# Performance work log

Hardware: AMD Instinct MI355X
Metric: run time of the kernel (lower is better)

The kernel has to match this reference:

```python
import jax, jax.numpy as jnp
import numpy as np

N_NODES = 50000
N_EDGES = 1600000
D_FEAT = 128
EMB = 32
HEADS = 4
SLOPE = 0.2  # PyG GATv2 default negative_slope


def setup_inputs() -> dict:
    key = jax.random.key(0)
    ks = jax.random.split(key, 12)
    H, C = HEADS, EMB
    hid = H * C  # concat output dim = 128

    def glorot(k, shape):
        fan_in, fan_out = shape[0], shape[-1] if len(shape) > 1 else shape[0]
        lim = jnp.sqrt(6.0 / (fan_in + fan_out)).astype(jnp.float32)
        return jax.random.uniform(k, shape, jnp.float32, -lim, lim)

    x = jax.random.normal(ks[0], (N_NODES, D_FEAT), jnp.float32)
    edge_index = jax.random.randint(ks[1], (2, N_EDGES), 0, N_NODES, jnp.int32).astype(jnp.int64)

    return {
        "x": x,
        "edge_index": edge_index,
        # layer 1: in D_FEAT -> H*C (separate source/target lins, share_weights=False)
        "W1_l": glorot(ks[2], (D_FEAT, hid)),
        "W1_r": glorot(ks[3], (D_FEAT, hid)),
        "att1": glorot(ks[4], (H, C)),
        "b1": jnp.zeros((hid,), jnp.float32),
        # layer 2: in H*C -> H*C
        "W2_l": glorot(ks[5], (hid, hid)),
        "W2_r": glorot(ks[6], (hid, hid)),
        "att2": glorot(ks[7], (H, C)),
        "b2": jnp.zeros((hid,), jnp.float32),
    }


def _gatv2_layer(x, src, dst, W_l, W_r, att, bias, n_nodes):
    H, C = att.shape
    xl = (x @ W_l).reshape(n_nodes, H, C)  # source-side transform
    xr = (x @ W_r).reshape(n_nodes, H, C)  # target-side transform
    # per-edge pre-activation: GATv2 applies LeakyReLU BEFORE the attention dot
    msg = xl[src] + xr[dst]                               # [E, H, C]
    e = jnp.einsum('ehc,hc->eh', jax.nn.leaky_relu(msg, SLOPE), att)  # [E, H]
    # numerically stable segment softmax over incoming edges of each dst node
    m = jax.ops.segment_max(e, dst, num_segments=n_nodes)  # [N, H]
    ex = jnp.exp(e - m[dst])
    denom = jax.ops.segment_sum(ex, dst, num_segments=n_nodes)  # [N, H]
    alpha = ex / (denom[dst] + 1e-16)                     # [E, H]
    out = jax.ops.segment_sum(alpha[:, :, None] * xl[src], dst, num_segments=n_nodes)
    return out.reshape(n_nodes, H * C) + bias


def reference(x, edge_index, W1_l, W1_r, att1, b1, W2_l, W2_r, att2, b2):
    n = x.shape[0]
    # PyG default add_self_loops=True: append (i -> i) for every node
    loop = jnp.arange(n, dtype=edge_index.dtype)
    src = jnp.concatenate([edge_index[0], loop])
    dst = jnp.concatenate([edge_index[1], loop])
    h = jax.nn.relu(_gatv2_layer(x, src, dst, W1_l, W1_r, att1, b1, n))
    h = jax.nn.relu(_gatv2_layer(h, src, dst, W2_l, W2_r, att2, b2, n))
    return h
```

## Files before the change

kernel.cpp:

```cpp
#include <hip/hip_runtime.h>

#define N_NODES 50000
#define N_EDGES 1600000
#define ET (N_EDGES + N_NODES)
#define DF 128
#define SLOPE 0.2f

#define NB 196
#define BCAP 10240
#define P1_CHUNK 4096

typedef __attribute__((ext_vector_type(8))) short bf16x8;
typedef __attribute__((ext_vector_type(4))) float floatx4;
typedef __attribute__((ext_vector_type(8))) _Float16 half8;
typedef __attribute__((ext_vector_type(2))) _Float16 half2v;

__device__ inline unsigned short f2bf(float v) {
    unsigned int u = __float_as_uint(v);
    u += 0x7FFF + ((u >> 16) & 1);
    return (unsigned short)(u >> 16);
}
__device__ inline void splitbf(float v, unsigned short& h, unsigned short& l) {
    h = f2bf(v);
    float hf = __uint_as_float((unsigned int)h << 16);
    l = f2bf(v - hf);
}

__global__ __launch_bounds__(256) void bin_wconv(
    const int* __restrict__ ei,
    const float* __restrict__ W0, const float* __restrict__ W1,
    const float* __restrict__ W2, const float* __restrict__ W3,
    unsigned short* __restrict__ Wh, unsigned short* __restrict__ Wl,
    int* __restrict__ g_count, int* __restrict__ bucket_mem)
{
    const int tid = threadIdx.x;
    if (blockIdx.x < 256) {
        int idx = blockIdx.x * 256 + tid;
        int m = idx >> 14, rem = idx & 16383;
        const float* W = (m == 0) ? W0 : (m == 1) ? W1 : (m == 2) ? W2 : W3;
        int c = rem >> 7, k = rem & 127;
        unsigned short h, l;
        splitbf(W[k * 128 + c], h, l);
        Wh[(size_t)m * 16384 + c * 128 + k] = h;
        Wl[(size_t)m * 16384 + c * 128 + k] = l;
    }

    __shared__ int cnt[NB], base[NB], cnt2[NB];
    for (int i = tid; i < NB; i += 256) { cnt[i] = 0; cnt2[i] = 0; }
    __syncthreads();

    const int e0 = blockIdx.x * P1_CHUNK;
    int srcv[16], dstv[16];
#pragma unroll
    for (int i = 0; i < 16; i++) {
        int eid = e0 + i * 256 + tid;
        int s = 0, d = -1;
        if (eid < ET) {
            if (eid < N_EDGES) { s = ei[eid]; d = ei[N_EDGES + eid]; }
            else               { s = d = eid - N_EDGES; }
        }
        srcv[i] = s; dstv[i] = d;
        if (d >= 0) atomicAdd(&cnt[d >> 8], 1);
    }
    __syncthreads();
    for (int i = tid; i < NB; i += 256)
        base[i] = (cnt[i] > 0) ? atomicAdd(&g_count[i], cnt[i]) : 0;
    __syncthreads();
#pragma unroll
    for (int i = 0; i < 16; i++) {
        int d = dstv[i];
        if (d >= 0) {
            int b = d >> 8;
            int r = atomicAdd(&cnt2[b], 1);
            int slot = base[b] + r;
            if (slot < BCAP)
                bucket_mem[(size_t)b * BCAP + slot] =
                    (srcv[i] & 0xFFFF) | ((d & 255) << 16);
        }
    }
}

__global__ __launch_bounds__(256) void csr_pass(const int* __restrict__ g_count,
                                                const int* __restrict__ bucket_mem,
                                                int* __restrict__ row_ptr,
                                                unsigned short* __restrict__ csr_src)
{
    __shared__ int sh_edges[BCAP];
    __shared__ int hist[256], offs[256], excl[256], cnt2[256];
    __shared__ int gsc[256];
    const int b = blockIdx.x, tid = threadIdx.x;

    gsc[tid] = (tid < NB) ? g_count[tid] : 0;
    __syncthreads();
    for (int d = 1; d < 256; d <<= 1) {
        int x = (tid >= d) ? gsc[tid - d] : 0;
        __syncthreads();
        gsc[tid] += x;
        __syncthreads();
    }
    const int base_csr = (b > 0) ? gsc[b - 1] : 0;

    int m = g_count[b]; if (m > BCAP) m = BCAP;
    hist[tid] = 0; cnt2[tid] = 0;
    __syncthreads();
    const int* bm = bucket_mem + (size_t)b * BCAP;
    for (int i = tid; i < m; i += 256) {
        int p = bm[i];
        sh_edges[i] = p;
        atomicAdd(&hist[(p >> 16) & 255], 1);
    }
    __syncthreads();
    offs[tid] = hist[tid]; __syncthreads();
    for (int d = 1; d < 256; d <<= 1) {
        int x = (tid >= d) ? offs[tid - d] : 0;
        __syncthreads();
        offs[tid] += x;
        __syncthreads();
    }
    excl[tid] = offs[tid] - hist[tid];
    const int node0 = b << 8;
    if (node0 + tid < N_NODES) row_ptr[node0 + tid] = base_csr + excl[tid];
    if (b == 0 && tid == 0) row_ptr[N_NODES] = ET;
    __syncthreads();
    for (int i = tid; i < m; i += 256) {
        int p = sh_edges[i];
        int dl = (p >> 16) & 255;
        int r = atomicAdd(&cnt2[dl], 1);
        csr_src[base_csr + excl[dl] + r] = (unsigned short)(p & 0xFFFF);
    }
}

__global__ __launch_bounds__(256) void gemm_mfma(
    const float* __restrict__ X,
    const unsigned short* __restrict__ WhL, const unsigned short* __restrict__ WlL,
    const unsigned short* __restrict__ WhR, const unsigned short* __restrict__ WlR,
    _Float16* __restrict__ outL, _Float16* __restrict__ outR, int M)
{
    __shared__ unsigned short xh[64 * 40], xl[64 * 40];
    __shared__ unsigned short whL[128 * 40], wlL[128 * 40];
    __shared__ unsigned short whR[128 * 40], wlR[128 * 40];

    const int t = threadIdx.x;
    const int row0 = blockIdx.x * 64;
    const int lane = t & 63, wv = t >> 6;
    const int lm = lane & 15, quad = lane >> 4;
    const int m0 = wv * 16;

    floatx4 accL[8], accR[8];
#pragma unroll
    for (int i = 0; i < 8; i++) { accL[i] = (floatx4)0.f; accR[i] = (floatx4)0.f; }

    const int sr = t >> 2;
    const int sc = (t & 3) * 8;
    const int wn = t >> 1;
    const int wkh = (t & 1) * 16;

    for (int kb = 0; kb < 128; kb += 32) {
        int xrow = row0 + sr; if (xrow >= M) xrow = M - 1;
        const float* xp = X + (size_t)xrow * DF + kb + sc;
        float4 v0 = *(const float4*)(xp);
        float4 v1 = *(const float4*)(xp + 4);
        ushort4 h0, h1, l0, l1;
        splitbf(v0.x, h0.x, l0.x); splitbf(v0.y, h0.y, l0.y);
        splitbf(v0.z, h0.z, l0.z); splitbf(v0.w, h0.w, l0.w);
        splitbf(v1.x, h1.x, l1.x); splitbf(v1.y, h1.y, l1.y);
        splitbf(v1.z, h1.z, l1.z); splitbf(v1.w, h1.w, l1.w);
        *(ushort4*)&xh[sr * 40 + sc]     = h0;
        *(ushort4*)&xh[sr * 40 + sc + 4] = h1;
        *(ushort4*)&xl[sr * 40 + sc]     = l0;
        *(ushort4*)&xl[sr * 40 + sc + 4] = l1;

        const size_t wofs = (size_t)wn * 128 + kb + wkh;
        {
            const uint4* p = (const uint4*)(WhL + wofs);
            uint4 a = p[0], b = p[1];
            *(uint4*)&whL[wn * 40 + wkh] = a; *(uint4*)&whL[wn * 40 + wkh + 8] = b;
        }
        {
            const uint4* p = (const uint4*)(WlL + wofs);
            uint4 a = p[0], b = p[1];
            *(uint4*)&wlL[wn * 40 + wkh] = a; *(uint4*)&wlL[wn * 40 + wkh + 8] = b;
        }
        {
            const uint4* p = (const uint4*)(WhR + wofs);
            uint4 a = p[0], b = p[1];
            *(uint4*)&whR[wn * 40 + wkh] = a; *(uint4*)&whR[wn * 40 + wkh + 8] = b;
        }
        {
            const uint4* p = (const uint4*)(WlR + wofs);
            uint4 a = p[0], b = p[1];
            *(uint4*)&wlR[wn * 40 + wkh] = a; *(uint4*)&wlR[wn * 40 + wkh + 8] = b;
        }
        __syncthreads();

        bf16x8 ahf = *(const bf16x8*)&xh[(m0 + lm) * 40 + quad * 8];
        bf16x8 alf = *(const bf16x8*)&xl[(m0 + lm) * 40 + quad * 8];
#pragma unroll
        for (int nt = 0; nt < 8; nt++) {
            const int bofs = (nt * 16 + lm) * 40 + quad * 8;
            bf16x8 bh = *(const bf16x8*)&whL[bofs];
            bf16x8 bl = *(const bf16x8*)&wlL[bofs];
            accL[nt] = __builtin_amdgcn_mfma_f32_16x16x32_bf16(ahf, bh, accL[nt], 0, 0, 0);
            accL[nt] = __builtin_amdgcn_mfma_f32_16x16x32_bf16(ahf, bl, accL[nt], 0, 0, 0);
            accL[nt] = __builtin_amdgcn_mfma_f32_16x16x32_bf16(alf, bh, accL[nt], 0, 0, 0);
            bf16x8 ch = *(const bf16x8*)&whR[bofs];
            bf16x8 cl = *(const bf16x8*)&wlR[bofs];
            accR[nt] = __builtin_amdgcn_mfma_f32_16x16x32_bf16(ahf, ch, accR[nt], 0, 0, 0);
            accR[nt] = __builtin_amdgcn_mfma_f32_16x16x32_bf16(ahf, cl, accR[nt], 0, 0, 0);
            accR[nt] = __builtin_amdgcn_mfma_f32_16x16x32_bf16(alf, ch, accR[nt], 0, 0, 0);
        }
        __syncthreads();
    }

#pragma unroll
    for (int nt = 0; nt < 8; nt++) {
        int col = (nt >> 2) * 64 + (nt & 3) * 16 + lm;
#pragma unroll
        for (int r = 0; r < 4; r++) {
            int gr = row0 + m0 + quad * 4 + r;
            if (gr < M) {
                size_t o = (size_t)gr * DF + col;
                outL[o] = (_Float16)accL[nt][r];
                outR[o] = (_Float16)accR[nt][r];
            }
        }
    }
}

__global__ __launch_bounds__(256) void fused_agg(
    const _Float16* __restrict__ XL, const _Float16* __restrict__ XR,
    const int* __restrict__ row_ptr, const unsigned short* __restrict__ csr_src,
    const float* __restrict__ att, const float* __restrict__ bias,
    float* __restrict__ out)
{
    const int t = threadIdx.x;
    const int wave = t >> 6, l = t & 63;
    const int g = l >> 4, gl = l & 15;
    const int n = blockIdx.x * 4 + wave;
    if (n >= N_NODES) return;
    const int beg = row_ptr[n], end = row_ptr[n + 1];

    const int c0 = gl * 8;
    half8 xrh = *(const half8*)(XR + (size_t)n * DF + c0);
    float4 at0 = *(const float4*)(att + c0);
    float4 at1 = *(const float4*)(att + c0 + 4);
    half2v a01 = { (_Float16)at0.x, (_Float16)at0.y };
    half2v a23 = { (_Float16)at0.z, (_Float16)at0.w };
    half2v a45 = { (_Float16)at1.x, (_Float16)at1.y };
    half2v a67 = { (_Float16)at1.z, (_Float16)at1.w };
    const half8 slp = { (_Float16)SLOPE, (_Float16)SLOPE, (_Float16)SLOPE, (_Float16)SLOPE,
                        (_Float16)SLOPE, (_Float16)SLOPE, (_Float16)SLOPE, (_Float16)SLOPE };

    float a0 = 0.f, a1 = 0.f, a2 = 0.f, a3 = 0.f;
    float a4 = 0.f, a5 = 0.f, a6 = 0.f, a7 = 0.f, den = 0.f;

    int eidx = beg + g;
    int s = (eidx < end) ? csr_src[eidx] : 0;
    half8 hv = *(const half8*)(XL + (size_t)s * DF + c0);

    for (int j = beg; j < end; j += 4) {
        int eidx_n = j + 4 + g;
        int s_n = (eidx_n < end) ? csr_src[eidx_n] : 0;
        half8 hv_n = *(const half8*)(XL + (size_t)s_n * DF + c0);

        half8 msg = hv + xrh;
        half8 lk  = __builtin_elementwise_max(msg, msg * slp);
        half2v m01 = { lk[0], lk[1] };
        half2v m23 = { lk[2], lk[3] };
        half2v m45 = { lk[4], lk[5] };
        half2v m67 = { lk[6], lk[7] };
        float p = __builtin_amdgcn_fdot2(m01, a01, 0.f, false);
        p = __builtin_amdgcn_fdot2(m23, a23, p, false);
        p = __builtin_amdgcn_fdot2(m45, a45, p, false);
        p = __builtin_amdgcn_fdot2(m67, a67, p, false);
        p += __shfl_xor(p, 1);
        p += __shfl_xor(p, 2);
        float e = (j + g < end) ? __expf(p) : 0.f;
        a0 += e * (float)hv[0]; a1 += e * (float)hv[1];
        a2 += e * (float)hv[2]; a3 += e * (float)hv[3];
        a4 += e * (float)hv[4]; a5 += e * (float)hv[5];
        a6 += e * (float)hv[6]; a7 += e * (float)hv[7];
        den += e;

        hv = hv_n;
    }

#define CMB(x) x += __shfl_xor(x, 16); x += __shfl_xor(x, 32);
    CMB(a0) CMB(a1) CMB(a2) CMB(a3) CMB(a4) CMB(a5) CMB(a6) CMB(a7) CMB(den)
#undef CMB

    if (g == 0) {
        float inv = 1.f / (den + 1e-16f);
        float4 b0 = *(const float4*)(bias + c0);
        float4 b1 = *(const float4*)(bias + c0 + 4);
        float4 o0, o1;
        o0.x = fmaxf(a0 * inv + b0.x, 0.f);
        o0.y = fmaxf(a1 * inv + b0.y, 0.f);
        o0.z = fmaxf(a2 * inv + b0.z, 0.f);
        o0.w = fmaxf(a3 * inv + b0.w, 0.f);
        o1.x = fmaxf(a4 * inv + b1.x, 0.f);
        o1.y = fmaxf(a5 * inv + b1.y, 0.f);
        o1.z = fmaxf(a6 * inv + b1.z, 0.f);
        o1.w = fmaxf(a7 * inv + b1.w, 0.f);
        float* op = out + (size_t)n * DF + c0;
        *(float4*)(op)     = o0;
        *(float4*)(op + 4) = o1;
    }
}

extern "C" void kernel_launch(void* const* d_in, const int* in_sizes, int n_in,
                              void* d_out, int out_size, void* d_ws, size_t ws_size,
                              hipStream_t stream)
{
    (void)in_sizes; (void)n_in; (void)out_size; (void)ws_size;

    const float* x    = (const float*)d_in[0];
    const int*   ei   = (const int*)d_in[1];
    const float* W1l  = (const float*)d_in[2];
    const float* W1r  = (const float*)d_in[3];
    const float* att1 = (const float*)d_in[4];
    const float* b1   = (const float*)d_in[5];
    const float* W2l  = (const float*)d_in[6];
    const float* W2r  = (const float*)d_in[7];
    const float* att2 = (const float*)d_in[8];
    const float* b2   = (const float*)d_in[9];
    float* out = (float*)d_out;

    char* ws = (char*)d_ws;
    size_t off = 0;
    const size_t NF = (size_t)N_NODES * DF * sizeof(float);
    _Float16* A = (_Float16*)(ws + off); off += NF / 2;
    _Float16* B = (_Float16*)(ws + off); off += NF / 2;
    float* C  = (float*)(ws + off); off += NF;
    int* bucket_mem  = (int*)(ws + off); off += (size_t)NB * BCAP * sizeof(int);
    int* g_count     = (int*)(ws + off); off += 256 * sizeof(int);
    int* row_ptr     = (int*)(ws + off); off += (size_t)(N_NODES + 1) * sizeof(int);
    unsigned short* csr_src = (unsigned short*)(ws + off);
    off += ((size_t)ET * sizeof(unsigned short) + 255) & ~(size_t)255;
    unsigned short* Wh = (unsigned short*)(ws + off); off += 4 * 16384 * sizeof(unsigned short);
    unsigned short* Wl = (unsigned short*)(ws + off); off += 4 * 16384 * sizeof(unsigned short);

    hipMemsetAsync(g_count, 0, 256 * sizeof(int), stream);
    bin_wconv<<<(ET + P1_CHUNK - 1) / P1_CHUNK, 256, 0, stream>>>(
        ei, W1l, W1r, W2l, W2r, Wh, Wl, g_count, bucket_mem);
    csr_pass<<<NB, 256, 0, stream>>>(g_count, bucket_mem, row_ptr, csr_src);

    dim3 gg((N_NODES + 63) / 64);
    dim3 ga((N_NODES + 3) / 4);

    gemm_mfma<<<gg, 256, 0, stream>>>(x, Wh, Wl, Wh + 16384, Wl + 16384, A, B, N_NODES);
    fused_agg<<<ga, 256, 0, stream>>>(A, B, row_ptr, csr_src, att1, b1, C);

    gemm_mfma<<<gg, 256, 0, stream>>>(C, Wh + 2 * 16384, Wl + 2 * 16384,
                                      Wh + 3 * 16384, Wl + 3 * 16384, A, B, N_NODES);
    fused_agg<<<ga, 256, 0, stream>>>(A, B, row_ptr, csr_src, att2, b2, out);
}
```

Measured before the change: 301.9 us.

## Merge layer-1 GEMM with edge binning, store hidden as fp16, unroll aggregation

Weight conversion now runs as its own small kernel that also zeroes the bucket counters, replacing the memset. The layer-1 GEMM and the edge-binning pass are merged into one launch whose blocks pick a role by block index, so the two independent jobs can run together. The layer-1 output is stored as fp16 rather than fp32 to halve its write and read traffic, at some cost in precision. The aggregation loop now processes two edge groups per iteration with a deeper prefetch to expose more memory parallelism.

```diff
diff --git a/kernel.cpp b/kernel.cpp
--- a/kernel.cpp
+++ b/kernel.cpp
@@ -9,6 +9,8 @@
 #define NB 196
 #define BCAP 10240
 #define P1_CHUNK 4096
+#define GEMM_BLOCKS ((N_NODES + 63) / 64)
+#define BIN_BLOCKS ((ET + P1_CHUNK - 1) / P1_CHUNK)
 
 typedef __attribute__((ext_vector_type(8))) short bf16x8;
 typedef __attribute__((ext_vector_type(4))) float floatx4;
@@ -26,122 +28,50 @@
     l = f2bf(v - hf);
 }
 
-__global__ __launch_bounds__(256) void bin_wconv(
-    const int* __restrict__ ei,
+__device__ __forceinline__ void load8f(const float* p, float* v) {
+    float4 a = *(const float4*)(p);
+    float4 b = *(const float4*)(p + 4);
+    v[0]=a.x; v[1]=a.y; v[2]=a.z; v[3]=a.w; v[4]=b.x; v[5]=b.y; v[6]=b.z; v[7]=b.w;
+}
+__device__ __forceinline__ void load8f(const _Float16* p, float* v) {
+    half8 h = *(const half8*)(p);
+#pragma unroll
+    for (int i = 0; i < 8; i++) v[i] = (float)h[i];
+}
+
+__global__ __launch_bounds__(256) void wconv4(
     const float* __restrict__ W0, const float* __restrict__ W1,
     const float* __restrict__ W2, const float* __restrict__ W3,
     unsigned short* __restrict__ Wh, unsigned short* __restrict__ Wl,
-    int* __restrict__ g_count, int* __restrict__ bucket_mem)
-{
-    const int tid = threadIdx.x;
-    if (blockIdx.x < 256) {
-        int idx = blockIdx.x * 256 + tid;
-        int m = idx >> 14, rem = idx & 16383;
-        const float* W = (m == 0) ? W0 : (m == 1) ? W1 : (m == 2) ? W2 : W3;
-        int c = rem >> 7, k = rem & 127;
-        unsigned short h, l;
-        splitbf(W[k * 128 + c], h, l);
-        Wh[(size_t)m * 16384 + c * 128 + k] = h;
-        Wl[(size_t)m * 16384 + c * 128 + k] = l;
-    }
-
-    __shared__ int cnt[NB], base[NB], cnt2[NB];
-    for (int i = tid; i < NB; i += 256) { cnt[i] = 0; cnt2[i] = 0; }
-    __syncthreads();
-
-    const int e0 = blockIdx.x * P1_CHUNK;
-    int srcv[16], dstv[16];
-#pragma unroll
-    for (int i = 0; i < 16; i++) {
-        int eid = e0 + i * 256 + tid;
-        int s = 0, d = -1;
-        if (eid < ET) {
-            if (eid < N_EDGES) { s = ei[eid]; d = ei[N_EDGES + eid]; }
-            else               { s = d = eid - N_EDGES; }
-        }
-        srcv[i] = s; dstv[i] = d;
-        if (d >= 0) atomicAdd(&cnt[d >> 8], 1);
-    }
-    __syncthreads();
-    for (int i = tid; i < NB; i += 256)
-        base[i] = (cnt[i] > 0) ? atomicAdd(&g_count[i], cnt[i]) : 0;
-    __syncthreads();
-#pragma unroll
-    for (int i = 0; i < 16; i++) {
-        int d = dstv[i];
-        if (d >= 0) {
-            int b = d >> 8;
-            int r = atomicAdd(&cnt2[b], 1);
-            int slot = base[b] + r;
-            if (slot < BCAP)
-                bucket_mem[(size_t)b * BCAP + slot] =
-                    (srcv[i] & 0xFFFF) | ((d & 255) << 16);
-        }
-    }
-}
-
-__global__ __launch_bounds__(256) void csr_pass(const int* __restrict__ g_count,
-                                                const int* __restrict__ bucket_mem,
-                                                int* __restrict__ row_ptr,
-                                                unsigned short* __restrict__ csr_src)
-{
-    __shared__ int sh_edges[BCAP];
-    __shared__ int hist[256], offs[256], excl[256], cnt2[256];
-    __shared__ int gsc[256];
-    const int b = blockIdx.x, tid = threadIdx.x;
-
-    gsc[tid] = (tid < NB) ? g_count[tid] : 0;
-    __syncthreads();
-    for (int d = 1; d < 256; d <<= 1) {
-        int x = (tid >= d) ? gsc[tid - d] : 0;
-        __syncthreads();
-        gsc[tid] += x;
-        __syncthreads();
-    }
-    const int base_csr = (b > 0) ? gsc[b - 1] : 0;
-
-    int m = g_count[b]; if (m > BCAP) m = BCAP;
-    hist[tid] = 0; cnt2[tid] = 0;
-    __syncthreads();
-    const int* bm = bucket_mem + (size_t)b * BCAP;
-    for (int i = tid; i < m; i += 256) {
-        int p = bm[i];
-        sh_edges[i] = p;
-        atomicAdd(&hist[(p >> 16) & 255], 1);
-    }
-    __syncthreads();
-    offs[tid] = hist[tid]; __syncthreads();
-    for (int d = 1; d < 256; d <<= 1) {
-        int x = (tid >= d) ? offs[tid - d] : 0;
-        __syncthreads();
-        offs[tid] += x;
-        __syncthreads();
-    }
-    excl[tid] = offs[tid] - hist[tid];
-    const int node0 = b << 8;
-    if (node0 + tid < N_NODES) row_ptr[node0 + tid] = base_csr + excl[tid];
-    if (b == 0 && tid == 0) row_ptr[N_NODES] = ET;
-    __syncthreads();
-    for (int i = tid; i < m; i += 256) {
-        int p = sh_edges[i];
-        int dl = (p >> 16) & 255;
-        int r = atomicAdd(&cnt2[dl], 1);
-        csr_src[base_csr + excl[dl] + r] = (unsigned short)(p & 0xFFFF);
-    }
-}
-
-__global__ __launch_bounds__(256) void gemm_mfma(
-    const float* __restrict__ X,
+    int* __restrict__ g_count)
+{
+    if (blockIdx.x == 0) g_count[threadIdx.x] = 0;
+    int idx = blockIdx.x * 256 + threadIdx.x;
+    int m = idx >> 14, rem = idx & 16383;
+    const float* W = (m == 0) ? W0 : (m == 1) ? W1 : (m == 2) ? W2 : W3;
+    int c = rem >> 7, k = rem & 127;
+    unsigned short h, l;
+    splitbf(W[k * 128 + c], h, l);
+    Wh[(size_t)m * 16384 + c * 128 + k] = h;
+    Wl[(size_t)m * 16384 + c * 128 + k] = l;
+}
+
+template<typename T>
+__device__ __forceinline__ void gemm_body(
+    int bid, const T* __restrict__ X,
     const unsigned short* __restrict__ WhL, const unsigned short* __restrict__ WlL,
     const unsigned short* __restrict__ WhR, const unsigned short* __restrict__ WlR,
-    _Float16* __restrict__ outL, _Float16* __restrict__ outR, int M)
-{
-    __shared__ unsigned short xh[64 * 40], xl[64 * 40];
-    __shared__ unsigned short whL[128 * 40], wlL[128 * 40];
-    __shared__ unsigned short whR[128 * 40], wlR[128 * 40];
+    _Float16* __restrict__ outL, _Float16* __restrict__ outR, int M, char* smem_)
+{
+    unsigned short* xh  = (unsigned short*)smem_;
+    unsigned short* xls = xh + 64 * 40;
+    unsigned short* whL = xls + 64 * 40;
+    unsigned short* wlL = whL + 128 * 40;
+    unsigned short* whR = wlL + 128 * 40;
+    unsigned short* wlR = whR + 128 * 40;
 
     const int t = threadIdx.x;
-    const int row0 = blockIdx.x * 64;
+    const int row0 = bid * 64;
     const int lane = t & 63, wv = t >> 6;
     const int lm = lane & 15, quad = lane >> 4;
     const int m0 = wv * 16;
@@ -157,18 +87,17 @@
 
     for (int kb = 0; kb < 128; kb += 32) {
         int xrow = row0 + sr; if (xrow >= M) xrow = M - 1;
-        const float* xp = X + (size_t)xrow * DF + kb + sc;
-        float4 v0 = *(const float4*)(xp);
-        float4 v1 = *(const float4*)(xp + 4);
+        float xv[8];
+        load8f(X + (size_t)xrow * DF + kb + sc, xv);
         ushort4 h0, h1, l0, l1;
-        splitbf(v0.x, h0.x, l0.x); splitbf(v0.y, h0.y, l0.y);
-        splitbf(v0.z, h0.z, l0.z); splitbf(v0.w, h0.w, l0.w);
-        splitbf(v1.x, h1.x, l1.x); splitbf(v1.y, h1.y, l1.y);
-        splitbf(v1.z, h1.z, l1.z); splitbf(v1.w, h1.w, l1.w);
-        *(ushort4*)&xh[sr * 40 + sc]     = h0;
-        *(ushort4*)&xh[sr * 40 + sc + 4] = h1;
-        *(ushort4*)&xl[sr * 40 + sc]     = l0;
-        *(ushort4*)&xl[sr * 40 + sc + 4] = l1;
+        splitbf(xv[0], h0.x, l0.x); splitbf(xv[1], h0.y, l0.y);
+        splitbf(xv[2], h0.z, l0.z); splitbf(xv[3], h0.w, l0.w);
+        splitbf(xv[4], h1.x, l1.x); splitbf(xv[5], h1.y, l1.y);
+        splitbf(xv[6], h1.z, l1.z); splitbf(xv[7], h1.w, l1.w);
+        *(ushort4*)&xh[sr * 40 + sc]      = h0;
+        *(ushort4*)&xh[sr * 40 + sc + 4]  = h1;
+        *(ushort4*)&xls[sr * 40 + sc]     = l0;
+        *(ushort4*)&xls[sr * 40 + sc + 4] = l1;
 
         const size_t wofs = (size_t)wn * 128 + kb + wkh;
         {
@@ -194,7 +123,7 @@
         __syncthreads();
 
         bf16x8 ahf = *(const bf16x8*)&xh[(m0 + lm) * 40 + quad * 8];
-        bf16x8 alf = *(const bf16x8*)&xl[(m0 + lm) * 40 + quad * 8];
+        bf16x8 alf = *(const bf16x8*)&xls[(m0 + lm) * 40 + quad * 8];
 #pragma unroll
         for (int nt = 0; nt < 8; nt++) {
             const int bofs = (nt * 16 + lm) * 40 + quad * 8;
@@ -227,11 +156,130 @@
     }
 }
 
+__device__ __forceinline__ void bin_body(
+    int bid, const int* __restrict__ ei,
+    int* __restrict__ g_count, int* __restrict__ bucket_mem, char* smem_)
+{
+    int* cnt  = (int*)smem_;
+    int* base = cnt + NB;
+    int* cnt2 = base + NB;
+    const int tid = threadIdx.x;
+
+    for (int i = tid; i < NB; i += 256) { cnt[i] = 0; cnt2[i] = 0; }
+    __syncthreads();
+
+    const int e0 = bid * P1_CHUNK;
+    int srcv[16], dstv[16];
+#pragma unroll
+    for (int i = 0; i < 16; i++) {
+        int eid = e0 + i * 256 + tid;
+        int s = 0, d = -1;
+        if (eid < ET) {
+            if (eid < N_EDGES) { s = ei[eid]; d = ei[N_EDGES + eid]; }
+            else               { s = d = eid - N_EDGES; }
+        }
+        srcv[i] = s; dstv[i] = d;
+        if (d >= 0) atomicAdd(&cnt[d >> 8], 1);
+    }
+    __syncthreads();
+    for (int i = tid; i < NB; i += 256)
+        base[i] = (cnt[i] > 0) ? atomicAdd(&g_count[i], cnt[i]) : 0;
+    __syncthreads();
+#pragma unroll
+    for (int i = 0; i < 16; i++) {
+        int d = dstv[i];
+        if (d >= 0) {
+            int b = d >> 8;
+            int r = atomicAdd(&cnt2[b], 1);
+            int slot = base[b] + r;
+            if (slot < BCAP)
+                bucket_mem[(size_t)b * BCAP + slot] =
+                    (srcv[i] & 0xFFFF) | ((d & 255) << 16);
+        }
+    }
+}
+
+__global__ __launch_bounds__(256) void gemm_bin(
+    const float* __restrict__ X,
+    const unsigned short* __restrict__ Wh, const unsigned short* __restrict__ Wl,
+    _Float16* __restrict__ outL, _Float16* __restrict__ outR,
+    const int* __restrict__ ei,
+    int* __restrict__ g_count, int* __restrict__ bucket_mem)
+{
+    __shared__ char smem[51200];
+    if (blockIdx.x < GEMM_BLOCKS)
+        gemm_body<float>(blockIdx.x, X, Wh, Wl, Wh + 16384, Wl + 16384,
+                         outL, outR, N_NODES, smem);
+    else
+        bin_body(blockIdx.x - GEMM_BLOCKS, ei, g_count, bucket_mem, smem);
+}
+
+__global__ __launch_bounds__(256) void gemm_f16(
+    const _Float16* __restrict__ X,
+    const unsigned short* __restrict__ Wh, const unsigned short* __restrict__ Wl,
+    _Float16* __restrict__ outL, _Float16* __restrict__ outR)
+{
+    __shared__ char smem[51200];
+    gemm_body<_Float16>(blockIdx.x, X, Wh, Wl, Wh + 16384, Wl + 16384,
+                        outL, outR, N_NODES, smem);
+}
+
+__global__ __launch_bounds__(256) void csr_pass(const int* __restrict__ g_count,
+                                                const int* __restrict__ bucket_mem,
+                                                int* __restrict__ row_ptr,
+                                                unsigned short* __restrict__ csr_src)
+{
+    __shared__ int sh_edges[BCAP];
+    __shared__ int hist[256], offs[256], excl[256], cnt2[256];
+    __shared__ int gsc[256];
+    const int b = blockIdx.x, tid = threadIdx.x;
+
+    gsc[tid] = (tid < NB) ? g_count[tid] : 0;
+    __syncthreads();
+    for (int d = 1; d < 256; d <<= 1) {
+        int x = (tid >= d) ? gsc[tid - d] : 0;
+        __syncthreads();
+        gsc[tid] += x;
+        __syncthreads();
+    }
+    const int base_csr = (b > 0) ? gsc[b - 1] : 0;
+
+    int m = g_count[b]; if (m > BCAP) m = BCAP;
+    hist[tid] = 0; cnt2[tid] = 0;
+    __syncthreads();
+    const int* bm = bucket_mem + (size_t)b * BCAP;
+    for (int i = tid; i < m; i += 256) {
+        int p = bm[i];
+        sh_edges[i] = p;
+        atomicAdd(&hist[(p >> 16) & 255], 1);
+    }
+    __syncthreads();
+    offs[tid] = hist[tid]; __syncthreads();
+    for (int d = 1; d < 256; d <<= 1) {
+        int x = (tid >= d) ? offs[tid - d] : 0;
+        __syncthreads();
+        offs[tid] += x;
+        __syncthreads();
+    }
+    excl[tid] = offs[tid] - hist[tid];
+    const int node0 = b << 8;
+    if (node0 + tid < N_NODES) row_ptr[node0 + tid] = base_csr + excl[tid];
+    if (b == 0 && tid == 0) row_ptr[N_NODES] = ET;
+    __syncthreads();
+    for (int i = tid; i < m; i += 256) {
+        int p = sh_edges[i];
+        int dl = (p >> 16) & 255;
+        int r = atomicAdd(&cnt2[dl], 1);
+        csr_src[base_csr + excl[dl] + r] = (unsigned short)(p & 0xFFFF);
+    }
+}
+
+template<typename TOut>
 __global__ __launch_bounds__(256) void fused_agg(
     const _Float16* __restrict__ XL, const _Float16* __restrict__ XR,
     const int* __restrict__ row_ptr, const unsigned short* __restrict__ csr_src,
     const float* __restrict__ att, const float* __restrict__ bias,
-    float* __restrict__ out)
+    TOut* __restrict__ out)
 {
     const int t = threadIdx.x;
     const int wave = t >> 6, l = t & 63;
@@ -254,36 +302,49 @@
     float a0 = 0.f, a1 = 0.f, a2 = 0.f, a3 = 0.f;
     float a4 = 0.f, a5 = 0.f, a6 = 0.f, a7 = 0.f, den = 0.f;
 
-    int eidx = beg + g;
-    int s = (eidx < end) ? csr_src[eidx] : 0;
-    half8 hv = *(const half8*)(XL + (size_t)s * DF + c0);
-
-    for (int j = beg; j < end; j += 4) {
-        int eidx_n = j + 4 + g;
-        int s_n = (eidx_n < end) ? csr_src[eidx_n] : 0;
-        half8 hv_n = *(const half8*)(XL + (size_t)s_n * DF + c0);
-
-        half8 msg = hv + xrh;
-        half8 lk  = __builtin_elementwise_max(msg, msg * slp);
-        half2v m01 = { lk[0], lk[1] };
-        half2v m23 = { lk[2], lk[3] };
-        half2v m45 = { lk[4], lk[5] };
-        half2v m67 = { lk[6], lk[7] };
-        float p = __builtin_amdgcn_fdot2(m01, a01, 0.f, false);
-        p = __builtin_amdgcn_fdot2(m23, a23, p, false);
-        p = __builtin_amdgcn_fdot2(m45, a45, p, false);
-        p = __builtin_amdgcn_fdot2(m67, a67, p, false);
-        p += __shfl_xor(p, 1);
-        p += __shfl_xor(p, 2);
-        float e = (j + g < end) ? __expf(p) : 0.f;
-        a0 += e * (float)hv[0]; a1 += e * (float)hv[1];
-        a2 += e * (float)hv[2]; a3 += e * (float)hv[3];
-        a4 += e * (float)hv[4]; a5 += e * (float)hv[5];
-        a6 += e * (float)hv[6]; a7 += e * (float)hv[7];
-        den += e;
-
-        hv = hv_n;
-    }
+    int e0i = beg + g;
+    int s0 = (e0i < end) ? csr_src[e0i] : 0;
+    half8 hv0 = *(const half8*)(XL + (size_t)s0 * DF + c0);
+    int e1i = beg + 4 + g;
+    int s1 = (e1i < end) ? csr_src[e1i] : 0;
+    half8 hv1 = *(const half8*)(XL + (size_t)s1 * DF + c0);
+
+#define EDGE_STEP(HV, EOK)                                                     \
+    {                                                                          \
+        half8 msg = HV + xrh;                                                  \
+        half8 lk  = __builtin_elementwise_max(msg, msg * slp);                 \
+        half2v m01 = { lk[0], lk[1] };                                         \
+        half2v m23 = { lk[2], lk[3] };                                         \
+        half2v m45 = { lk[4], lk[5] };                                         \
+        half2v m67 = { lk[6], lk[7] };                                         \
+        float p = __builtin_amdgcn_fdot2(m01, a01, 0.f, false);                \
+        p = __builtin_amdgcn_fdot2(m23, a23, p, false);                        \
+        p = __builtin_amdgcn_fdot2(m45, a45, p, false);                        \
+        p = __builtin_amdgcn_fdot2(m67, a67, p, false);                        \
+        p += __shfl_xor(p, 1);                                                 \
+        p += __shfl_xor(p, 2);                                                 \
+        float e = (EOK) ? __expf(p) : 0.f;                                     \
+        a0 += e * (float)HV[0]; a1 += e * (float)HV[1];                        \
+        a2 += e * (float)HV[2]; a3 += e * (float)HV[3];                        \
+        a4 += e * (float)HV[4]; a5 += e * (float)HV[5];                        \
+        a6 += e * (float)HV[6]; a7 += e * (float)HV[7];                        \
+        den += e;                                                              \
+    }
+
+    for (int j = beg; j < end; j += 8) {
+        int en0 = j + 8 + g;
+        int sn0 = (en0 < end) ? csr_src[en0] : 0;
+        half8 hn0 = *(const half8*)(XL + (size_t)sn0 * DF + c0);
+        int en1 = j + 12 + g;
+        int sn1 = (en1 < end) ? csr_src[en1] : 0;
+        half8 hn1 = *(const half8*)(XL + (size_t)sn1 * DF + c0);
+
+        EDGE_STEP(hv0, (j + g < end))
+        EDGE_STEP(hv1, (j + 4 + g < end))
+
+        hv0 = hn0; hv1 = hn1;
+    }
+#undef EDGE_STEP
 
 #define CMB(x) x += __shfl_xor(x, 16); x += __shfl_xor(x, 32);
     CMB(a0) CMB(a1) CMB(a2) CMB(a3) CMB(a4) CMB(a5) CMB(a6) CMB(a7) CMB(den)
@@ -293,18 +354,25 @@
         float inv = 1.f / (den + 1e-16f);
         float4 b0 = *(const float4*)(bias + c0);
         float4 b1 = *(const float4*)(bias + c0 + 4);
-        float4 o0, o1;
-        o0.x = fmaxf(a0 * inv + b0.x, 0.f);
-        o0.y = fmaxf(a1 * inv + b0.y, 0.f);
-        o0.z = fmaxf(a2 * inv + b0.z, 0.f);
-        o0.w = fmaxf(a3 * inv + b0.w, 0.f);
-        o1.x = fmaxf(a4 * inv + b1.x, 0.f);
-        o1.y = fmaxf(a5 * inv + b1.y, 0.f);
-        o1.z = fmaxf(a6 * inv + b1.z, 0.f);
-        o1.w = fmaxf(a7 * inv + b1.w, 0.f);
-        float* op = out + (size_t)n * DF + c0;
-        *(float4*)(op)     = o0;
-        *(float4*)(op + 4) = o1;
+        float o[8];
+        o[0] = fmaxf(a0 * inv + b0.x, 0.f);
+        o[1] = fmaxf(a1 * inv + b0.y, 0.f);
+        o[2] = fmaxf(a2 * inv + b0.z, 0.f);
+        o[3] = fmaxf(a3 * inv + b0.w, 0.f);
+        o[4] = fmaxf(a4 * inv + b1.x, 0.f);
+        o[5] = fmaxf(a5 * inv + b1.y, 0.f);
+        o[6] = fmaxf(a6 * inv + b1.z, 0.f);
+        o[7] = fmaxf(a7 * inv + b1.w, 0.f);
+        TOut* op = out + (size_t)n * DF + c0;
+        if constexpr (sizeof(TOut) == 2) {
+            half8 hv;
+#pragma unroll
+            for (int i = 0; i < 8; i++) hv[i] = (_Float16)o[i];
+            *(half8*)op = hv;
+        } else {
+            *(float4*)(op)     = make_float4(o[0], o[1], o[2], o[3]);
+            *(float4*)(op + 4) = make_float4(o[4], o[5], o[6], o[7]);
+        }
     }
 }
 
@@ -331,7 +399,7 @@
     const size_t NF = (size_t)N_NODES * DF * sizeof(float);
     _Float16* A = (_Float16*)(ws + off); off += NF / 2;
     _Float16* B = (_Float16*)(ws + off); off += NF / 2;
-    float* C  = (float*)(ws + off); off += NF;
+    _Float16* C = (_Float16*)(ws + off); off += NF / 2;
     int* bucket_mem  = (int*)(ws + off); off += (size_t)NB * BCAP * sizeof(int);
     int* g_count     = (int*)(ws + off); off += 256 * sizeof(int);
     int* row_ptr     = (int*)(ws + off); off += (size_t)(N_NODES + 1) * sizeof(int);
@@ -340,18 +408,15 @@
     unsigned short* Wh = (unsigned short*)(ws + off); off += 4 * 16384 * sizeof(unsigned short);
     unsigned short* Wl = (unsigned short*)(ws + off); off += 4 * 16384 * sizeof(unsigned short);
 
-    hipMemsetAsync(g_count, 0, 256 * sizeof(int), stream);
-    bin_wconv<<<(ET + P1_CHUNK - 1) / P1_CHUNK, 256, 0, stream>>>(
-        ei, W1l, W1r, W2l, W2r, Wh, Wl, g_count, bucket_mem);
+    wconv4<<<256, 256, 0, stream>>>(W1l, W1r, W2l, W2r, Wh, Wl, g_count);
+
+    gemm_bin<<<GEMM_BLOCKS + BIN_BLOCKS, 256, 0, stream>>>(
+        x, Wh, Wl, A, B, ei, g_count, bucket_mem);
     csr_pass<<<NB, 256, 0, stream>>>(g_count, bucket_mem, row_ptr, csr_src);
-
-    dim3 gg((N_NODES + 63) / 64);
-    dim3 ga((N_NODES + 3) / 4);
-
-    gemm_mfma<<<gg, 256, 0, stream>>>(x, Wh, Wl, Wh + 16384, Wl + 16384, A, B, N_NODES);
-    fused_agg<<<ga, 256, 0, stream>>>(A, B, row_ptr, csr_src, att1, b1, C);
-
-    gemm_mfma<<<gg, 256, 0, stream>>>(C, Wh + 2 * 16384, Wl + 2 * 16384,
-                                      Wh + 3 * 16384, Wl + 3 * 16384, A, B, N_NODES);
-    fused_agg<<<ga, 256, 0, stream>>>(A, B, row_ptr, csr_src, att2, b2, out);
-}
+    fused_agg<_Float16><<<(N_NODES + 3) / 4, 256, 0, stream>>>(
+        A, B, row_ptr, csr_src, att1, b1, C);
+
+    gemm_f16<<<GEMM_BLOCKS, 256, 0, stream>>>(C, Wh + 2 * 16384, Wl + 2 * 16384, A, B);
+    fused_agg<float><<<(N_NODES + 3) / 4, 256, 0, stream>>>(
+        A, B, row_ptr, csr_src, att2, b2, out);
+}
```

Measured after the change: 287.1 us. -4.9%, faster.
